# Kernel tuning notes

Hardware: AMD Instinct MI355X
Metric: run time of the kernel (lower is better)

The kernel has to match this reference:

```python
import jax, jax.numpy as jnp
import numpy as np

# Blade ordering for G(3,0,1): [1, e0, e1, e2, e3, e01, e02, e03, e12, e13, e23, e012, e013, e023, e123, e0123]
_GRADES = np.array([0, 1, 1, 1, 1, 2, 2, 2, 2, 2, 2, 3, 3, 3, 3, 4])
# e0-wedge map: blade without e0 -> e0 ^ blade (all signs +1 with this ordering)
_E0_MAP = {0: 1, 2: 5, 3: 6, 4: 7, 8: 11, 9: 12, 10: 13, 14: 15}


def _make_basis():
    """9 Pin(3,0,1)-equivariant linear maps on 16-dim multivectors: B[9,16,16]."""
    B = np.zeros((9, 16, 16), dtype=np.float32)
    for g in range(5):  # grade projections
        for i, gi in enumerate(_GRADES):
            if gi == g:
                B[g, i, i] = 1.0
    for g in range(4):  # e0-wedge per grade
        for src, dst in _E0_MAP.items():
            if _GRADES[src] == g:
                B[5 + g, dst, src] = 1.0
    return jnp.asarray(B)


def setup_inputs() -> dict:
    key = jax.random.key(0)
    ks = jax.random.split(key, 9)
    n_parent, stride = 65536, 2
    in_mv, out_mv, in_s, out_s = 32, 32, 64, 64
    n_child = n_parent * stride
    return {
        "x_mv": jax.random.normal(ks[0], (n_parent, in_mv, 16), jnp.float32),
        "x_s": jax.random.normal(ks[1], (n_parent, in_s), jnp.float32),
        "skip_mv": jax.random.normal(ks[2], (n_child, out_mv, 16), jnp.float32),
        "skip_s": jax.random.normal(ks[3], (n_child, out_s), jnp.float32),
        "w_mv": jax.random.normal(ks[4], (out_mv, in_mv, 9), jnp.float32) * 0.1,
        "w_s2mv": jax.random.normal(ks[5], (out_mv, in_s), jnp.float32) * 0.1,
        "w_mv2s": jax.random.normal(ks[6], (out_s, in_mv), jnp.float32) * 0.1,
        "w_s2s": jax.random.normal(ks[7], (out_s, in_s), jnp.float32) * 0.1,
        "b_s": jax.random.normal(ks[8], (out_s,), jnp.float32) * 0.1,
        "stride": stride,
    }


def reference(x_mv, x_s, skip_mv, skip_s, w_mv, w_s2mv, w_mv2s, w_s2s, b_s, stride):
    B = _make_basis()
    # Propagate parents to children (repeat_interleave along node dim)
    xp_mv = jnp.repeat(x_mv, stride, axis=0)   # [Nc, in_mv, 16]
    xp_s = jnp.repeat(x_s, stride, axis=0)     # [Nc, in_s]
    # EquiLinear: combine 9 basis maps with channel-mixing weights
    W = jnp.einsum('oib,bjk->oijk', w_mv, B)   # [out_mv, in_mv, 16, 16]
    out_mv = jnp.einsum('nik,oijk->noj', xp_mv, W)  # [Nc, out_mv, 16]
    # scalars -> scalar (grade-0) component of multivectors
    out_mv = out_mv.at[:, :, 0].add(xp_s @ w_s2mv.T)
    # mv scalar component + scalars -> output scalars
    out_s = xp_mv[:, :, 0] @ w_mv2s.T + xp_s @ w_s2s.T + b_s
    # Residual add onto skip connection (children features)
    return skip_mv + out_mv, skip_s + out_s
```

## Files before the change

### kernel.cpp

```cpp
#include <hip/hip_runtime.h>

typedef __attribute__((ext_vector_type(8))) short bf16x8;
typedef __attribute__((ext_vector_type(4))) float f32x4;

#define THR 256
#define PBLK 32

__device__ __forceinline__ unsigned int bf_rne(float f) {
    unsigned int u = __float_as_uint(f);
    u += 0x7fffu + ((u >> 16) & 1u);
    return u >> 16;
}

#define MFMA(A, B, C) __builtin_amdgcn_mfma_f32_16x16x32_bf16((A), (B), (C), 0, 0, 0)

#define XB(ti, j, pl, slot) ((ti) * 8320 + (j) * 520 + (pl) * 32 + (slot) * 8)
#define YPS 520
#define YSS 68

#define NSLOT 13

__global__ __launch_bounds__(THR) void build_frags(
    const float* __restrict__ w_mv, const float* __restrict__ w_s2mv,
    const float* __restrict__ w_mv2s, const float* __restrict__ w_s2s,
    bf16x8* __restrict__ wsf)
{
    const int t = threadIdx.x;
    const int lane = t & 63;
    const int wid  = t >> 6;
    const int h   = wid & 1;
    const int jh  = wid >> 1;
    const int col = lane & 15;
    const int g4  = lane >> 4;
    const int kb  = g4 * 8;
    const int oo  = h * 16 + col;

    bf16x8 z;
    #pragma unroll
    for (int e = 0; e < 8; ++e) z[e] = 0;

    #pragma unroll
    for (int gg = 0; gg < 3; ++gg) {
        int b = 2 * jh + gg;
        bf16x8 v = z;
        #pragma unroll
        for (int e = 0; e < 8; ++e)
            v[e] = (short)bf_rne(w_mv[oo * 288 + (kb + e) * 9 + b]);
        wsf[gg * THR + t] = v;
    }
    #pragma unroll
    for (int ww = 0; ww < 2; ++ww) {
        int b = 5 + 2 * jh + ww;
        bf16x8 v = z;
        #pragma unroll
        for (int e = 0; e < 8; ++e)
            v[e] = (short)bf_rne(w_mv[oo * 288 + (kb + e) * 9 + b]);
        wsf[(3 + ww) * THR + t] = v;
    }
    if (jh == 0) {
        #pragma unroll
        for (int c = 0; c < 2; ++c) {
            bf16x8 v = z;
            #pragma unroll
            for (int e = 0; e < 8; ++e)
                v[e] = (short)bf_rne(w_mv2s[((2 * h + c) * 16 + col) * 32 + kb + e]);
            wsf[(5 + c) * THR + t] = v;
        }
        #pragma unroll
        for (int kk = 0; kk < 2; ++kk) {
            bf16x8 v = z;
            #pragma unroll
            for (int e = 0; e < 8; ++e)
                v[e] = (short)bf_rne(w_s2mv[oo * 64 + kk * 32 + kb + e]);
            wsf[(7 + kk) * THR + t] = v;
            #pragma unroll
            for (int c = 0; c < 2; ++c) {
                bf16x8 u = z;
                #pragma unroll
                for (int e = 0; e < 8; ++e)
                    u[e] = (short)bf_rne(w_s2s[((2 * h + c) * 16 + col) * 64 + kk * 32 + kb + e]);
                wsf[(9 + kk * 2 + c) * THR + t] = u;
            }
        }
    } else {
        #pragma unroll
        for (int s = 5; s < NSLOT; ++s) wsf[s * THR + t] = z;
    }
}

__global__ __launch_bounds__(THR) void equi_mfma(
    const float* __restrict__ x_mv,
    const float* __restrict__ x_s,
    const float* __restrict__ skip_mv,
    const float* __restrict__ skip_s,
    const bf16x8* __restrict__ wsf,
    const float* __restrict__ b_s,
    float* __restrict__ out_mv,
    float* __restrict__ out_s,
    int n_parent, int stride)
{
    __shared__ char smem[37632];
    unsigned short* xb  = (unsigned short*)smem;
    unsigned short* xsb = (unsigned short*)(smem + 33280);
    float* y  = (float*)smem;
    float* ys = (float*)(smem + 33280);

    const int t  = threadIdx.x;
    const int p0 = blockIdx.x * PBLK;

    {
        const int p   = t >> 3;
        const int ig2 = (t >> 2) & 1;
        const int jq  = t & 3;
        const int ti  = p >> 4, pl = p & 15;
        const float4* xg = (const float4*)(x_mv + (size_t)p0 * 512);
        const int base = p * 128 + ig2 * 64 + jq;
        bf16x8 acc[4][2];
        #pragma unroll
        for (int s = 0; s < 16; ++s) {
            float4 v = xg[base + s * 4];
            int igl = s >> 3, e = s & 7;
            acc[0][igl][e] = (short)bf_rne(v.x);
            acc[1][igl][e] = (short)bf_rne(v.y);
            acc[2][igl][e] = (short)bf_rne(v.z);
            acc[3][igl][e] = (short)bf_rne(v.w);
        }
        #pragma unroll
        for (int jo = 0; jo < 4; ++jo)
            #pragma unroll
            for (int igl = 0; igl < 2; ++igl) {
                int ig = ig2 * 2 + igl;
                int slot = ig ^ (pl & 3) ^ jq;
                *(bf16x8*)&xb[XB(ti, jq * 4 + jo, pl, slot)] = acc[jo][igl];
            }
        const int q = t & 7;
        const int ps = t >> 3;
        const int tis = ps >> 4, pls = ps & 15;
        const float4* xsg = (const float4*)(x_s + (size_t)p0 * 64);
        float4 v0 = xsg[ps * 16 + q * 2 + 0];
        float4 v1 = xsg[ps * 16 + q * 2 + 1];
        bf16x8 sv;
        sv[0] = (short)bf_rne(v0.x); sv[1] = (short)bf_rne(v0.y);
        sv[2] = (short)bf_rne(v0.z); sv[3] = (short)bf_rne(v0.w);
        sv[4] = (short)bf_rne(v1.x); sv[5] = (short)bf_rne(v1.y);
        sv[6] = (short)bf_rne(v1.z); sv[7] = (short)bf_rne(v1.w);
        *(bf16x8*)&xsb[((tis * 16 + pls) * 8 + (q ^ (pls & 7))) * 8] = sv;
    }

    const int lane = t & 63;
    const int wid  = t >> 6;
    const int h   = wid & 1;
    const int jh  = wid >> 1;
    const int col = lane & 15;
    const int g4  = lane >> 4;
    const int oo  = h * 16 + col;

    bf16x8 Bg[3], Bw[2], Bm2s[2], Bs2mv[2], Bs2s[2][2];
    Bg[0]      = wsf[0 * THR + t];
    Bg[1]      = wsf[1 * THR + t];
    Bg[2]      = wsf[2 * THR + t];
    Bw[0]      = wsf[3 * THR + t];
    Bw[1]      = wsf[4 * THR + t];
    Bm2s[0]    = wsf[5 * THR + t];
    Bm2s[1]    = wsf[6 * THR + t];
    Bs2mv[0]   = wsf[7 * THR + t];
    Bs2mv[1]   = wsf[8 * THR + t];
    Bs2s[0][0] = wsf[9 * THR + t];
    Bs2s[0][1] = wsf[10 * THR + t];
    Bs2s[1][0] = wsf[11 * THR + t];
    Bs2s[1][1] = wsf[12 * THR + t];

    __syncthreads();

    f32x4 cj[2][8];
    f32x4 cs[2][2];
    #pragma unroll
    for (int ti = 0; ti < 2; ++ti) {
        #pragma unroll
        for (int jj = 0; jj < 8; ++jj) cj[ti][jj] = (f32x4){0.f, 0.f, 0.f, 0.f};
        cs[ti][0] = (f32x4){0.f, 0.f, 0.f, 0.f};
        cs[ti][1] = (f32x4){0.f, 0.f, 0.f, 0.f};
    }
    const int prow = col;

    if (jh == 0) {
        #pragma unroll
        for (int ti = 0; ti < 2; ++ti) {
            bf16x8 A0;
            #pragma unroll
            for (int jj = 0; jj < 8; ++jj) {
                int slot = g4 ^ (prow & 3) ^ (jj >> 2);
                bf16x8 A = *(const bf16x8*)&xb[XB(ti, jj, prow, slot)];
                if (jj == 0)      cj[ti][0] = MFMA(A, Bg[0], cj[ti][0]);
                else if (jj < 5)  cj[ti][jj] = MFMA(A, Bg[1], cj[ti][jj]);
                else              cj[ti][jj] = MFMA(A, Bg[2], cj[ti][jj]);
                if (jj == 0) { cj[ti][1] = MFMA(A, Bw[0], cj[ti][1]); A0 = A; }
                else if (jj == 2) cj[ti][5] = MFMA(A, Bw[1], cj[ti][5]);
                else if (jj == 3) cj[ti][6] = MFMA(A, Bw[1], cj[ti][6]);
                else if (jj == 4) cj[ti][7] = MFMA(A, Bw[1], cj[ti][7]);
            }
            cs[ti][0] = MFMA(A0, Bm2s[0], cs[ti][0]);
            cs[ti][1] = MFMA(A0, Bm2s[1], cs[ti][1]);
            #pragma unroll
            for (int kk = 0; kk < 2; ++kk) {
                const unsigned short* sp = &xsb[((ti * 16 + prow) * 8 + ((kk * 4 + g4) ^ (prow & 7))) * 8];
                bf16x8 Axs = *(const bf16x8*)sp;
                cj[ti][0] = MFMA(Axs, Bs2mv[kk], cj[ti][0]);
                cs[ti][0] = MFMA(Axs, Bs2s[kk][0], cs[ti][0]);
                cs[ti][1] = MFMA(Axs, Bs2s[kk][1], cs[ti][1]);
            }
        }
    } else {
        #pragma unroll
        for (int ti = 0; ti < 2; ++ti) {
            #pragma unroll
            for (int jj = 0; jj < 8; ++jj) {
                int j = 8 + jj;
                int slot = g4 ^ (prow & 3) ^ (j >> 2);
                bf16x8 A = *(const bf16x8*)&xb[XB(ti, j, prow, slot)];
                if (jj < 3)       cj[ti][jj] = MFMA(A, Bg[0], cj[ti][jj]);
                else if (jj < 7)  cj[ti][jj] = MFMA(A, Bg[1], cj[ti][jj]);
                else              cj[ti][jj] = MFMA(A, Bg[2], cj[ti][jj]);
                if (jj == 0)      cj[ti][3] = MFMA(A, Bw[0], cj[ti][3]);
                else if (jj == 1) cj[ti][4] = MFMA(A, Bw[0], cj[ti][4]);
                else if (jj == 2) cj[ti][5] = MFMA(A, Bw[0], cj[ti][5]);
                else if (jj == 6) cj[ti][7] = MFMA(A, Bw[1], cj[ti][7]);
            }
        }
    }

    #pragma unroll
    for (int hf = 0; hf < 2; ++hf) {
        __syncthreads();
        #pragma unroll
        for (int r = 0; r < 4; ++r) {
            int p = g4 * 4 + r;
            #pragma unroll
            for (int q4 = 0; q4 < 2; ++q4) {
                int jqg  = jh * 2 + q4;
                int quad = jqg ^ (oo & 3) ^ g4;
                float4 w;
                w.x = cj[hf][q4 * 4 + 0][r];
                w.y = cj[hf][q4 * 4 + 1][r];
                w.z = cj[hf][q4 * 4 + 2][r];
                w.w = cj[hf][q4 * 4 + 3][r];
                *(float4*)&y[p * YPS + oo * 16 + quad * 4] = w;
            }
        }
        if (jh == 0) {
            #pragma unroll
            for (int c = 0; c < 2; ++c)
                #pragma unroll
                for (int r = 0; r < 4; ++r)
                    ys[(g4 * 4 + r) * YSS + (2 * h + c) * 16 + col] = cs[hf][c][r];
        }
        __syncthreads();

        const int cbase = (p0 + hf * 16) * stride;
        const float4* sk4 = (const float4*)skip_mv;
        float4* om4 = (float4*)out_mv;
        const float4* sks4 = (const float4*)skip_s;
        float4* os4 = (float4*)out_s;
        const float4* bs4 = (const float4*)b_s;

        if (stride == 2) {
            #pragma unroll
            for (int bt = 0; bt < 4; ++bt) {
                size_t gidx[4];
                float4 sv[4], yv[4];
                #pragma unroll
                for (int u = 0; u < 4; ++u) {
                    int id = t + (bt * 4 + u) * THR;
                    int child = id >> 7, rem = id & 127;
                    int o = rem >> 2, q = rem & 3;
                    int ph = child >> 1;
                    int quad = q ^ (o & 3) ^ (ph >> 2);
                    gidx[u] = (size_t)(cbase + child) * 128 + rem;
                    sv[u] = sk4[gidx[u]];
                    yv[u] = *(const float4*)&y[ph * YPS + o * 16 + quad * 4];
                }
                #pragma unroll
                for (int u = 0; u < 4; ++u)
                    om4[gidx[u]] = make_float4(sv[u].x + yv[u].x, sv[u].y + yv[u].y,
                                               sv[u].z + yv[u].z, sv[u].w + yv[u].w);
            }
            {
                size_t gidx[2];
                float4 sv[2], av[2];
                #pragma unroll
                for (int u = 0; u < 2; ++u) {
                    int id = t + u * THR;
                    int child = id >> 4, ch4 = id & 15;
                    int ph = child >> 1;
                    float4 ad = *(const float4*)&ys[ph * YSS + ch4 * 4];
                    float4 bb = bs4[ch4];
                    gidx[u] = (size_t)(cbase + child) * 16 + ch4;
                    sv[u] = sks4[gidx[u]];
                    av[u] = make_float4(ad.x + bb.x, ad.y + bb.y, ad.z + bb.z, ad.w + bb.w);
                }
                #pragma unroll
                for (int u = 0; u < 2; ++u)
                    os4[gidx[u]] = make_float4(sv[u].x + av[u].x, sv[u].y + av[u].y,
                                               sv[u].z + av[u].z, sv[u].w + av[u].w);
            }
        } else {
            const int totmv = 16 * stride * 128;
            for (int id = t; id < totmv; id += THR) {
                int child = id >> 7, rem = id & 127;
                int o = rem >> 2, q = rem & 3;
                int ph = child / stride;
                int quad = q ^ (o & 3) ^ (ph >> 2);
                float4 ad = *(const float4*)&y[ph * YPS + o * 16 + quad * 4];
                size_t gi = (size_t)(cbase + child) * 128 + rem;
                float4 s = sk4[gi];
                om4[gi] = make_float4(s.x + ad.x, s.y + ad.y, s.z + ad.z, s.w + ad.w);
            }
            const int tots = 16 * stride * 16;
            for (int id = t; id < tots; id += THR) {
                int child = id >> 4, ch4 = id & 15;
                int ph = child / stride;
                float4 ad = *(const float4*)&ys[ph * YSS + ch4 * 4];
                float4 bb = bs4[ch4];
                size_t gi = (size_t)(cbase + child) * 16 + ch4;
                float4 s = sks4[gi];
                os4[gi] = make_float4(s.x + ad.x + bb.x, s.y + ad.y + bb.y,
                                      s.z + ad.z + bb.z, s.w + ad.w + bb.w);
            }
        }
    }
}

__global__ __launch_bounds__(256) void equi_tail(
    const float* __restrict__ x_mv, const float* __restrict__ x_s,
    const float* __restrict__ skip_mv, const float* __restrict__ skip_s,
    const float* __restrict__ w_mv, const float* __restrict__ w_s2mv,
    const float* __restrict__ w_mv2s, const float* __restrict__ w_s2s,
    const float* __restrict__ b_s,
    float* __restrict__ out_mv, float* __restrict__ out_s,
    int pstart, int n_parent, int stride)
{
    int idx = blockIdx.x * blockDim.x + threadIdx.x;
    int o = idx & 31, pr = idx >> 5;
    int p = pstart + pr;
    if (p >= n_parent) return;
    float a[16];
    #pragma unroll
    for (int j = 0; j < 16; ++j) a[j] = 0.f;
    float s0 = 0.f, s1 = 0.f;
    const float4* xg = (const float4*)(x_mv + (size_t)p * 512);
    for (int i = 0; i < 32; ++i) {
        float4 X0 = xg[i * 4 + 0], X1 = xg[i * 4 + 1], X2 = xg[i * 4 + 2], X3 = xg[i * 4 + 3];
        const float* wp = &w_mv[o * 288 + i * 9];
        float w0 = wp[0], w1 = wp[1], w2 = wp[2], w3 = wp[3], w4 = wp[4];
        float w5 = wp[5], w6 = wp[6], w7 = wp[7], w8 = wp[8];
        a[0] += X0.x * w0;  a[1] += X0.y * w1 + X0.x * w5;
        a[2] += X0.z * w1;  a[3] += X0.w * w1;  a[4] += X1.x * w1;
        a[5] += X1.y * w2 + X0.z * w6;  a[6] += X1.z * w2 + X0.w * w6;
        a[7] += X1.w * w2 + X1.x * w6;  a[8] += X2.x * w2;
        a[9] += X2.y * w2;  a[10] += X2.z * w2;
        a[11] += X2.w * w3 + X2.x * w7;  a[12] += X3.x * w3 + X2.y * w7;
        a[13] += X3.y * w3 + X2.z * w7;  a[14] += X3.z * w3;
        a[15] += X3.w * w4 + X3.z * w8;
        s0 += X0.x * w_mv2s[o * 32 + i];
        s1 += X0.x * w_mv2s[(o + 32) * 32 + i];
    }
    for (int sc = 0; sc < 64; ++sc) {
        float xv = x_s[(size_t)p * 64 + sc];
        a[0] += xv * w_s2mv[o * 64 + sc];
        s0 += xv * w_s2s[o * 64 + sc];
        s1 += xv * w_s2s[(o + 32) * 64 + sc];
    }
    s0 += b_s[o]; s1 += b_s[o + 32];
    for (int r = 0; r < stride; ++r) {
        size_t c = (size_t)p * stride + r;
        const float4* sk = (const float4*)(skip_mv + c * 512 + o * 16);
        float4* om = (float4*)(out_mv + c * 512 + o * 16);
        float4 k0 = sk[0], k1 = sk[1], k2 = sk[2], k3 = sk[3];
        om[0] = make_float4(k0.x + a[0],  k0.y + a[1],  k0.z + a[2],  k0.w + a[3]);
        om[1] = make_float4(k1.x + a[4],  k1.y + a[5],  k1.z + a[6],  k1.w + a[7]);
        om[2] = make_float4(k2.x + a[8],  k2.y + a[9],  k2.z + a[10], k2.w + a[11]);
        om[3] = make_float4(k3.x + a[12], k3.y + a[13], k3.z + a[14], k3.w + a[15]);
        out_s[c * 64 + o]      = skip_s[c * 64 + o] + s0;
        out_s[c * 64 + o + 32] = skip_s[c * 64 + o + 32] + s1;
    }
}

extern "C" void kernel_launch(void* const* d_in, const int* in_sizes, int n_in,
                              void* d_out, int out_size, void* d_ws, size_t ws_size,
                              hipStream_t stream) {
    const float* x_mv    = (const float*)d_in[0];
    const float* x_s     = (const float*)d_in[1];
    const float* skip_mv = (const float*)d_in[2];
    const float* skip_s  = (const float*)d_in[3];
    const float* w_mv    = (const float*)d_in[4];
    const float* w_s2mv  = (const float*)d_in[5];
    const float* w_mv2s  = (const float*)d_in[6];
    const float* w_s2s   = (const float*)d_in[7];
    const float* b_s     = (const float*)d_in[8];

    const int n_parent = in_sizes[0] / 512;
    const int n_child  = in_sizes[2] / 512;
    const int stride   = n_child / n_parent;

    float* out_mv = (float*)d_out;
    float* out_s  = out_mv + (size_t)n_child * 512;
    bf16x8* wsf = (bf16x8*)d_ws;

    build_frags<<<1, THR, 0, stream>>>(w_mv, w_s2mv, w_mv2s, w_s2s, wsf);

    const int full = n_parent >> 5;
    const int rem  = n_parent & 31;
    if (full > 0)
        equi_mfma<<<full, THR, 0, stream>>>(
            x_mv, x_s, skip_mv, skip_s, wsf, b_s,
            out_mv, out_s, n_parent, stride);
    if (rem > 0) {
        int thr = rem * 32;
        int blk = (thr + 255) / 256;
        equi_tail<<<blk, 256, 0, stream>>>(
            x_mv, x_s, skip_mv, skip_s, w_mv, w_s2mv, w_mv2s, w_s2s, b_s,
            out_mv, out_s, full * 32, n_parent, stride);
    }
}
```

Baseline: 155.2 us.

## Stage outputs as bf16 in LDS and write both halves in one pass

```diff
diff --git a/kernel.cpp b/kernel.cpp
--- a/kernel.cpp
+++ b/kernel.cpp
@@ -11,6 +11,11 @@
     u += 0x7fffu + ((u >> 16) & 1u);
     return u >> 16;
 }
+__device__ __forceinline__ unsigned int pack2(float a, float b) {
+    return bf_rne(a) | (bf_rne(b) << 16);
+}
+__device__ __forceinline__ float bf_lo(unsigned int u) { return __uint_as_float(u << 16); }
+__device__ __forceinline__ float bf_hi(unsigned int u) { return __uint_as_float(u & 0xffff0000u); }
 
 #define MFMA(A, B, C) __builtin_amdgcn_mfma_f32_16x16x32_bf16((A), (B), (C), 0, 0, 0)
 
@@ -102,8 +107,8 @@
     __shared__ char smem[37632];
     unsigned short* xb  = (unsigned short*)smem;
     unsigned short* xsb = (unsigned short*)(smem + 33280);
-    float* y  = (float*)smem;
-    float* ys = (float*)(smem + 33280);
+    unsigned short* yb  = (unsigned short*)smem;
+    unsigned short* ysb = (unsigned short*)(smem + 33280);
 
     const int t  = threadIdx.x;
     const int p0 = blockIdx.x * PBLK;
@@ -229,103 +234,106 @@
         }
     }
 
-    #pragma unroll
-    for (int hf = 0; hf < 2; ++hf) {
-        __syncthreads();
+    __syncthreads();
+    #pragma unroll
+    for (int ti = 0; ti < 2; ++ti)
         #pragma unroll
         for (int r = 0; r < 4; ++r) {
-            int p = g4 * 4 + r;
+            int p = ti * 16 + g4 * 4 + r;
             #pragma unroll
             for (int q4 = 0; q4 < 2; ++q4) {
                 int jqg  = jh * 2 + q4;
-                int quad = jqg ^ (oo & 3) ^ g4;
-                float4 w;
-                w.x = cj[hf][q4 * 4 + 0][r];
-                w.y = cj[hf][q4 * 4 + 1][r];
-                w.z = cj[hf][q4 * 4 + 2][r];
-                w.w = cj[hf][q4 * 4 + 3][r];
-                *(float4*)&y[p * YPS + oo * 16 + quad * 4] = w;
-            }
-        }
-        if (jh == 0) {
+                int quad = jqg ^ (oo & 3) ^ (col >> 2) ^ g4;
+                uint2 w;
+                w.x = pack2(cj[ti][q4 * 4 + 0][r], cj[ti][q4 * 4 + 1][r]);
+                w.y = pack2(cj[ti][q4 * 4 + 2][r], cj[ti][q4 * 4 + 3][r]);
+                *(uint2*)&yb[p * YPS + oo * 16 + quad * 4] = w;
+            }
+        }
+    if (jh == 0) {
+        #pragma unroll
+        for (int ti = 0; ti < 2; ++ti)
             #pragma unroll
             for (int c = 0; c < 2; ++c)
                 #pragma unroll
                 for (int r = 0; r < 4; ++r)
-                    ys[(g4 * 4 + r) * YSS + (2 * h + c) * 16 + col] = cs[hf][c][r];
-        }
-        __syncthreads();
-
-        const int cbase = (p0 + hf * 16) * stride;
-        const float4* sk4 = (const float4*)skip_mv;
-        float4* om4 = (float4*)out_mv;
-        const float4* sks4 = (const float4*)skip_s;
-        float4* os4 = (float4*)out_s;
-        const float4* bs4 = (const float4*)b_s;
-
-        if (stride == 2) {
-            #pragma unroll
-            for (int bt = 0; bt < 4; ++bt) {
-                size_t gidx[4];
-                float4 sv[4], yv[4];
-                #pragma unroll
-                for (int u = 0; u < 4; ++u) {
-                    int id = t + (bt * 4 + u) * THR;
-                    int child = id >> 7, rem = id & 127;
-                    int o = rem >> 2, q = rem & 3;
-                    int ph = child >> 1;
-                    int quad = q ^ (o & 3) ^ (ph >> 2);
-                    gidx[u] = (size_t)(cbase + child) * 128 + rem;
-                    sv[u] = sk4[gidx[u]];
-                    yv[u] = *(const float4*)&y[ph * YPS + o * 16 + quad * 4];
-                }
-                #pragma unroll
-                for (int u = 0; u < 4; ++u)
-                    om4[gidx[u]] = make_float4(sv[u].x + yv[u].x, sv[u].y + yv[u].y,
-                                               sv[u].z + yv[u].z, sv[u].w + yv[u].w);
-            }
-            {
-                size_t gidx[2];
-                float4 sv[2], av[2];
-                #pragma unroll
-                for (int u = 0; u < 2; ++u) {
-                    int id = t + u * THR;
-                    int child = id >> 4, ch4 = id & 15;
-                    int ph = child >> 1;
-                    float4 ad = *(const float4*)&ys[ph * YSS + ch4 * 4];
-                    float4 bb = bs4[ch4];
-                    gidx[u] = (size_t)(cbase + child) * 16 + ch4;
-                    sv[u] = sks4[gidx[u]];
-                    av[u] = make_float4(ad.x + bb.x, ad.y + bb.y, ad.z + bb.z, ad.w + bb.w);
-                }
-                #pragma unroll
-                for (int u = 0; u < 2; ++u)
-                    os4[gidx[u]] = make_float4(sv[u].x + av[u].x, sv[u].y + av[u].y,
-                                               sv[u].z + av[u].z, sv[u].w + av[u].w);
-            }
-        } else {
-            const int totmv = 16 * stride * 128;
-            for (int id = t; id < totmv; id += THR) {
+                    ysb[(ti * 16 + g4 * 4 + r) * YSS + (2 * h + c) * 16 + col] =
+                        (unsigned short)bf_rne(cs[ti][c][r]);
+    }
+    __syncthreads();
+
+    const int cbase = p0 * stride;
+    const float4* sk4 = (const float4*)skip_mv;
+    float4* om4 = (float4*)out_mv;
+    const float4* sks4 = (const float4*)skip_s;
+    float4* os4 = (float4*)out_s;
+    const float4* bs4 = (const float4*)b_s;
+
+    if (stride == 2) {
+        #pragma unroll
+        for (int bt = 0; bt < 4; ++bt) {
+            size_t gidx[8];
+            float4 sv[8];
+            uint2  yv[8];
+            #pragma unroll
+            for (int u = 0; u < 8; ++u) {
+                int id = t + (bt * 8 + u) * THR;
                 int child = id >> 7, rem = id & 127;
                 int o = rem >> 2, q = rem & 3;
-                int ph = child / stride;
-                int quad = q ^ (o & 3) ^ (ph >> 2);
-                float4 ad = *(const float4*)&y[ph * YPS + o * 16 + quad * 4];
-                size_t gi = (size_t)(cbase + child) * 128 + rem;
-                float4 s = sk4[gi];
-                om4[gi] = make_float4(s.x + ad.x, s.y + ad.y, s.z + ad.z, s.w + ad.w);
-            }
-            const int tots = 16 * stride * 16;
-            for (int id = t; id < tots; id += THR) {
+                int ph = child >> 1;
+                int quad = q ^ (o & 3) ^ ((o >> 2) & 3) ^ ((ph >> 2) & 3);
+                gidx[u] = (size_t)(cbase + child) * 128 + rem;
+                sv[u] = sk4[gidx[u]];
+                yv[u] = *(const uint2*)&yb[ph * YPS + o * 16 + quad * 4];
+            }
+            #pragma unroll
+            for (int u = 0; u < 8; ++u)
+                om4[gidx[u]] = make_float4(sv[u].x + bf_lo(yv[u].x), sv[u].y + bf_hi(yv[u].x),
+                                           sv[u].z + bf_lo(yv[u].y), sv[u].w + bf_hi(yv[u].y));
+        }
+        {
+            size_t gidx[4];
+            float4 sv[4], av[4];
+            #pragma unroll
+            for (int u = 0; u < 4; ++u) {
+                int id = t + u * THR;
                 int child = id >> 4, ch4 = id & 15;
-                int ph = child / stride;
-                float4 ad = *(const float4*)&ys[ph * YSS + ch4 * 4];
+                int ph = child >> 1;
+                uint2 yv = *(const uint2*)&ysb[ph * YSS + ch4 * 4];
                 float4 bb = bs4[ch4];
-                size_t gi = (size_t)(cbase + child) * 16 + ch4;
-                float4 s = sks4[gi];
-                os4[gi] = make_float4(s.x + ad.x + bb.x, s.y + ad.y + bb.y,
-                                      s.z + ad.z + bb.z, s.w + ad.w + bb.w);
-            }
+                av[u] = make_float4(bf_lo(yv.x) + bb.x, bf_hi(yv.x) + bb.y,
+                                    bf_lo(yv.y) + bb.z, bf_hi(yv.y) + bb.w);
+                gidx[u] = (size_t)(cbase + child) * 16 + ch4;
+                sv[u] = sks4[gidx[u]];
+            }
+            #pragma unroll
+            for (int u = 0; u < 4; ++u)
+                os4[gidx[u]] = make_float4(sv[u].x + av[u].x, sv[u].y + av[u].y,
+                                           sv[u].z + av[u].z, sv[u].w + av[u].w);
+        }
+    } else {
+        const int totmv = PBLK * stride * 128;
+        for (int id = t; id < totmv; id += THR) {
+            int child = id >> 7, rem = id & 127;
+            int o = rem >> 2, q = rem & 3;
+            int ph = child / stride;
+            int quad = q ^ (o & 3) ^ ((o >> 2) & 3) ^ ((ph >> 2) & 3);
+            uint2 yv = *(const uint2*)&yb[ph * YPS + o * 16 + quad * 4];
+            size_t gi = (size_t)(cbase + child) * 128 + rem;
+            float4 s = sk4[gi];
+            om4[gi] = make_float4(s.x + bf_lo(yv.x), s.y + bf_hi(yv.x),
+                                  s.z + bf_lo(yv.y), s.w + bf_hi(yv.y));
+        }
+        const int tots = PBLK * stride * 16;
+        for (int id = t; id < tots; id += THR) {
+            int child = id >> 4, ch4 = id & 15;
+            int ph = child / stride;
+            uint2 yv = *(const uint2*)&ysb[ph * YSS + ch4 * 4];
+            float4 bb = bs4[ch4];
+            size_t gi = (size_t)(cbase + child) * 16 + ch4;
+            float4 s = sks4[gi];
+            os4[gi] = make_float4(s.x + bf_lo(yv.x) + bb.x, s.y + bf_hi(yv.x) + bb.y,
+                                  s.z + bf_lo(yv.y) + bb.z, s.w + bf_hi(yv.y) + bb.w);
         }
     }
 }
```

New measurement: 153.8 us. Within noise of the previous version (-0.9%).
